# Performance work log

Measured on AMD Instinct MI355X. Metric: run time of the kernel, lower is better.

The kernel has to match this reference:

```python
import jax, jax.numpy as jnp
import numpy as np

USER_SIZE = 100000
ITEM_SIZE = 100000
EMBED = 64
BATCH = 16384
A = 0.2  # history-pooling mixing coefficient (self.a in the torch module)


def setup_inputs() -> dict:
    key = jax.random.key(0)
    ks = jax.random.split(key, 16)
    d = {}
    # index inputs
    names = ["user", "item", "pre1", "pre2", "pre3", "pre4", "pre5"]
    for i, n in enumerate(names):
        vocab = USER_SIZE if n == "user" else ITEM_SIZE
        d[n] = jax.random.randint(ks[i], (BATCH,), 0, vocab, dtype=jnp.int32)
    # embedding tables (Linear(vocab, embed) weight transposed => (vocab, embed))
    d["Wu"] = jax.random.normal(ks[7], (USER_SIZE, EMBED), jnp.float32) * (1.0 / np.sqrt(USER_SIZE + EMBED))
    d["bu"] = jnp.zeros((EMBED,), jnp.float32)
    d["Wi"] = jax.random.normal(ks[8], (ITEM_SIZE, EMBED), jnp.float32) * (1.0 / np.sqrt(ITEM_SIZE + EMBED))
    d["bi"] = jnp.zeros((EMBED,), jnp.float32)
    # MLP: 2E -> 2E -> E -> 1 (torch Linear weight layout: (out, in))
    d["W1"] = jax.random.normal(ks[9], (2 * EMBED, 2 * EMBED), jnp.float32) * (1.0 / np.sqrt(2 * EMBED))
    d["b1"] = jnp.zeros((2 * EMBED,), jnp.float32)
    d["W2"] = jax.random.normal(ks[10], (EMBED, 2 * EMBED), jnp.float32) * (1.0 / np.sqrt(2 * EMBED))
    d["b2"] = jnp.zeros((EMBED,), jnp.float32)
    d["W3"] = jax.random.normal(ks[11], (1, EMBED), jnp.float32) * (1.0 / np.sqrt(EMBED))
    d["b3"] = jnp.zeros((1,), jnp.float32)
    return d


def reference(user, item, pre1, pre2, pre3, pre4, pre5,
              Wu, bu, Wi, bi, W1, b1, W2, b2, W3, b3):
    # one-hot @ Linear == row-gather from the (vocab, embed) table + bias
    eu = jax.nn.relu(Wu[user] + bu)                     # [B, E]
    ei = jax.nn.relu(Wi[item] + bi)                     # [B, E]
    pres = jnp.stack([pre1, pre2, pre3, pre4, pre5], 1) # [B, 5]
    ep = jax.nn.relu(Wi[pres] + bi)                     # [B, 5, E]
    # attention scores: dot(item_embed, each history embed), softmax over 5
    w = jnp.einsum("be,bke->bk", ei, ep)                # [B, 5]
    z = jax.nn.softmax(w, axis=1)                       # same math as exp/sum (stable)
    pum = jnp.einsum("bk,bke->be", z, ep)               # [B, E]
    pu = eu + A * pum
    x = jnp.concatenate([pu, ei], axis=-1)              # [B, 2E]
    h = jax.nn.relu(x @ W1.T + b1)
    h = jax.nn.relu(h @ W2.T + b2)
    out = h @ W3.T + b3                                 # [B, 1]
    return jax.nn.sigmoid(out).reshape(-1)              # [B]
```

## Files before the change

### kernel.cpp

```cpp
#include <hip/hip_runtime.h>
#include <hip/hip_bf16.h>
#include <math.h>

#define EMBED 64
#define BATCH 16384
#define TB 32
#define LDX 136

typedef __attribute__((ext_vector_type(8))) short short8;
typedef __attribute__((ext_vector_type(4))) float f32x4;

__device__ inline void store_bf16x4(__hip_bfloat16* dst, float4 v) {
    __hip_bfloat16 tmp[4];
    tmp[0] = __float2bfloat16(v.x); tmp[1] = __float2bfloat16(v.y);
    tmp[2] = __float2bfloat16(v.z); tmp[3] = __float2bfloat16(v.w);
    *reinterpret_cast<ushort4*>(dst) = *reinterpret_cast<ushort4*>(tmp);
}

__device__ inline short8 load_w_bf16(const float* p) {
    const float4 lo = reinterpret_cast<const float4*>(p)[0];
    const float4 hi = reinterpret_cast<const float4*>(p)[1];
    __hip_bfloat16 tb[8];
    tb[0] = __float2bfloat16(lo.x); tb[1] = __float2bfloat16(lo.y);
    tb[2] = __float2bfloat16(lo.z); tb[3] = __float2bfloat16(lo.w);
    tb[4] = __float2bfloat16(hi.x); tb[5] = __float2bfloat16(hi.y);
    tb[6] = __float2bfloat16(hi.z); tb[7] = __float2bfloat16(hi.w);
    return *reinterpret_cast<short8*>(tb);
}

__device__ inline void attn_one(float4 eu_r, float4 ei_r, float4 ep[5],
                                float4 bu4, float4 bi4,
                                __hip_bfloat16* xrow) {
    float4 eu, ei;
    eu.x = fmaxf(eu_r.x + bu4.x, 0.0f); eu.y = fmaxf(eu_r.y + bu4.y, 0.0f);
    eu.z = fmaxf(eu_r.z + bu4.z, 0.0f); eu.w = fmaxf(eu_r.w + bu4.w, 0.0f);
    ei.x = fmaxf(ei_r.x + bi4.x, 0.0f); ei.y = fmaxf(ei_r.y + bi4.y, 0.0f);
    ei.z = fmaxf(ei_r.z + bi4.z, 0.0f); ei.w = fmaxf(ei_r.w + bi4.w, 0.0f);

    float w[5];
    #pragma unroll
    for (int k = 0; k < 5; ++k) {
        ep[k].x = fmaxf(ep[k].x + bi4.x, 0.0f);
        ep[k].y = fmaxf(ep[k].y + bi4.y, 0.0f);
        ep[k].z = fmaxf(ep[k].z + bi4.z, 0.0f);
        ep[k].w = fmaxf(ep[k].w + bi4.w, 0.0f);
        w[k] = ei.x * ep[k].x + ei.y * ep[k].y + ei.z * ep[k].z + ei.w * ep[k].w;
    }

    #pragma unroll
    for (int k = 0; k < 5; ++k) {
        float v = w[k];
        v += __shfl_xor(v, 1, 64);
        v += __shfl_xor(v, 2, 64);
        v += __shfl_xor(v, 4, 64);
        v += __shfl_xor(v, 8, 64);
        w[k] = v;
    }

    float m = w[0];
    #pragma unroll
    for (int k = 1; k < 5; ++k) m = fmaxf(m, w[k]);
    float z[5], s = 0.0f;
    #pragma unroll
    for (int k = 0; k < 5; ++k) { z[k] = __expf(w[k] - m); s += z[k]; }
    const float scale = 0.2f / s;

    float4 pum = {0.0f, 0.0f, 0.0f, 0.0f};
    #pragma unroll
    for (int k = 0; k < 5; ++k) {
        pum.x += z[k] * ep[k].x; pum.y += z[k] * ep[k].y;
        pum.z += z[k] * ep[k].z; pum.w += z[k] * ep[k].w;
    }
    float4 pu;
    pu.x = eu.x + scale * pum.x; pu.y = eu.y + scale * pum.y;
    pu.z = eu.z + scale * pum.z; pu.w = eu.w + scale * pum.w;

    const int el = (threadIdx.x & 63) & 15;
    store_bf16x4(&xrow[el * 4], pu);
    store_bf16x4(&xrow[64 + el * 4], ei);
}

__global__ __launch_bounds__(256, 2) void ncf_fused(
    const int* __restrict__ user, const int* __restrict__ item,
    const int* __restrict__ p1, const int* __restrict__ p2,
    const int* __restrict__ p3, const int* __restrict__ p4, const int* __restrict__ p5,
    const float* __restrict__ Wu, const float* __restrict__ bu,
    const float* __restrict__ Wi, const float* __restrict__ bi,
    const float* __restrict__ W1, const float* __restrict__ b1v,
    const float* __restrict__ W2, const float* __restrict__ b2v,
    const float* __restrict__ W3, const float* __restrict__ b3,
    float* __restrict__ out)
{
    __shared__ __align__(16) __hip_bfloat16 xs [TB * LDX];
    __shared__ __align__(16) __hip_bfloat16 h1s[TB * LDX];
    __shared__ __align__(16) float          h2s[TB * 68];

    const int t    = threadIdx.x;
    const int lane = t & 63;
    const int wv   = t >> 6;
    const int blk  = blockIdx.x;

    const int fr = lane & 15;
    const int kg = lane >> 4;
    const int n0 = wv * 32;
    const int n2 = wv * 16;

    const int sub = lane >> 4;
    const int el  = lane & 15;
    const int b0  = wv * 4 + sub;
    const int b1  = 16 + b0;
    const int gb0 = blk * TB + b0;
    const int gb1 = blk * TB + b1;

    const int iu0 = user[gb0], ii0 = item[gb0];
    const int iu1 = user[gb1], ii1 = item[gb1];
    int ip0[5], ip1[5];
    ip0[0] = p1[gb0]; ip0[1] = p2[gb0]; ip0[2] = p3[gb0]; ip0[3] = p4[gb0]; ip0[4] = p5[gb0];
    ip1[0] = p1[gb1]; ip1[1] = p2[gb1]; ip1[2] = p3[gb1]; ip1[3] = p4[gb1]; ip1[4] = p5[gb1];

    const float4 eu_r0 = reinterpret_cast<const float4*>(&Wu[(size_t)iu0 * EMBED])[el];
    const float4 ei_r0 = reinterpret_cast<const float4*>(&Wi[(size_t)ii0 * EMBED])[el];
    const float4 eu_r1 = reinterpret_cast<const float4*>(&Wu[(size_t)iu1 * EMBED])[el];
    const float4 ei_r1 = reinterpret_cast<const float4*>(&Wi[(size_t)ii1 * EMBED])[el];
    float4 ep0[5], ep1[5];
    #pragma unroll
    for (int k = 0; k < 5; ++k) {
        ep0[k] = reinterpret_cast<const float4*>(&Wi[(size_t)ip0[k] * EMBED])[el];
        ep1[k] = reinterpret_cast<const float4*>(&Wi[(size_t)ip1[k] * EMBED])[el];
    }

    short8 b1f[2][4];
    #pragma unroll
    for (int tile = 0; tile < 2; ++tile)
        #pragma unroll
        for (int kc = 0; kc < 4; ++kc)
            b1f[tile][kc] = load_w_bf16(&W1[(n0 + tile * 16 + fr) * 128 + kc * 32 + kg * 8]);

    const float4 bu4 = reinterpret_cast<const float4*>(bu)[el];
    const float4 bi4 = reinterpret_cast<const float4*>(bi)[el];

    attn_one(eu_r0, ei_r0, ep0, bu4, bi4, &xs[b0 * LDX]);
    attn_one(eu_r1, ei_r1, ep1, bu4, bi4, &xs[b1 * LDX]);

    __syncthreads();

    {
        const float bb0 = b1v[n0 + fr];
        const float bb1 = b1v[n0 + 16 + fr];

        #pragma unroll
        for (int mt = 0; mt < 2; ++mt) {
            short8 a[4];
            #pragma unroll
            for (int kc = 0; kc < 4; ++kc)
                a[kc] = *reinterpret_cast<const short8*>(
                    &xs[(mt * 16 + fr) * LDX + kc * 32 + kg * 8]);

            f32x4 c0 = {bb0, bb0, bb0, bb0};
            f32x4 c1 = {bb1, bb1, bb1, bb1};
            #pragma unroll
            for (int kc = 0; kc < 4; ++kc) {
                c0 = __builtin_amdgcn_mfma_f32_16x16x32_bf16(a[kc], b1f[0][kc], c0, 0, 0, 0);
                c1 = __builtin_amdgcn_mfma_f32_16x16x32_bf16(a[kc], b1f[1][kc], c1, 0, 0, 0);
            }

            #pragma unroll
            for (int r = 0; r < 4; ++r) {
                const int row = mt * 16 + kg * 4 + r;
                h1s[row * LDX + n0 + fr]      = __float2bfloat16(fmaxf(c0[r], 0.0f));
                h1s[row * LDX + n0 + 16 + fr] = __float2bfloat16(fmaxf(c1[r], 0.0f));
            }
        }
    }

    short8 b2f[4];
    #pragma unroll
    for (int kc = 0; kc < 4; ++kc)
        b2f[kc] = load_w_bf16(&W2[(n2 + fr) * 128 + kc * 32 + kg * 8]);

    __syncthreads();

    {
        const float bb2 = b2v[n2 + fr];

        #pragma unroll
        for (int mt = 0; mt < 2; ++mt) {
            short8 a2[4];
            #pragma unroll
            for (int kc = 0; kc < 4; ++kc)
                a2[kc] = *reinterpret_cast<const short8*>(
                    &h1s[(mt * 16 + fr) * LDX + kc * 32 + kg * 8]);

            f32x4 c2 = {bb2, bb2, bb2, bb2};
            #pragma unroll
            for (int kc = 0; kc < 4; ++kc)
                c2 = __builtin_amdgcn_mfma_f32_16x16x32_bf16(a2[kc], b2f[kc], c2, 0, 0, 0);

            #pragma unroll
            for (int r = 0; r < 4; ++r)
                h2s[(mt * 16 + kg * 4 + r) * 68 + n2 + fr] = fmaxf(c2[r], 0.0f);
        }
    }

    __syncthreads();

    {
        const int bl = wv * 8 + (lane >> 3);
        const int q  = lane & 7;
        const float4* w3p = reinterpret_cast<const float4*>(&W3[q * 8]);
        const float4* hp  = reinterpret_cast<const float4*>(&h2s[bl * 68 + q * 8]);
        const float4 w0 = w3p[0], w1 = w3p[1];
        const float4 h0 = hp[0],  h1 = hp[1];
        float acc = h0.x * w0.x + h0.y * w0.y + h0.z * w0.z + h0.w * w0.w
                  + h1.x * w1.x + h1.y * w1.y + h1.z * w1.z + h1.w * w1.w;
        acc += __shfl_xor(acc, 1, 64);
        acc += __shfl_xor(acc, 2, 64);
        acc += __shfl_xor(acc, 4, 64);
        if (q == 0)
            out[blk * TB + bl] = 1.0f / (1.0f + __expf(-(acc + b3[0])));
    }
}

extern "C" void kernel_launch(void* const* d_in, const int* in_sizes, int n_in,
                              void* d_out, int out_size, void* d_ws, size_t ws_size,
                              hipStream_t stream) {
    const int*   user = (const int*)  d_in[0];
    const int*   item = (const int*)  d_in[1];
    const int*   p1   = (const int*)  d_in[2];
    const int*   p2   = (const int*)  d_in[3];
    const int*   p3   = (const int*)  d_in[4];
    const int*   p4   = (const int*)  d_in[5];
    const int*   p5   = (const int*)  d_in[6];
    const float* Wu   = (const float*)d_in[7];
    const float* bu   = (const float*)d_in[8];
    const float* Wi   = (const float*)d_in[9];
    const float* bi   = (const float*)d_in[10];
    const float* W1   = (const float*)d_in[11];
    const float* b1   = (const float*)d_in[12];
    const float* W2   = (const float*)d_in[13];
    const float* b2   = (const float*)d_in[14];
    const float* W3   = (const float*)d_in[15];
    const float* b3   = (const float*)d_in[16];
    float* out = (float*)d_out;

    hipLaunchKernelGGL(ncf_fused, dim3(BATCH / TB), dim3(256), 0, stream,
                       user, item, p1, p2, p3, p4, p5,
                       Wu, bu, Wi, bi, W1, b1, W2, b2, W3, b3, out);
}
```

Before: 15.30 us.

## Double batch tile to 64 rows with 512-thread blocks and remap MFMA work

Raises the batch tile per block from 32 to 64 and the block size to 512 threads (8 waves). Each wave now computes one 16-column slice of layer 1 across four row tiles, and layer 2 is split by row tile and column pair. The aim is to amortise the per-block fp32-to-bf16 conversion of W1/W2 fragments over twice as many rows and to halve the block count. The cost is fewer blocks (256) on a large GPU, which may reduce parallelism and latency hiding during the gathers. The layer-3 section is not shown, so its mapping for 64 rows cannot be checked.

```diff
diff --git a/kernel.cpp b/kernel.cpp
--- a/kernel.cpp
+++ b/kernel.cpp
@@ -4,7 +4,7 @@
 
 #define EMBED 64
 #define BATCH 16384
-#define TB 32
+#define TB 64
 #define LDX 136
 
 typedef __attribute__((ext_vector_type(8))) short short8;
@@ -80,7 +80,7 @@
     store_bf16x4(&xrow[64 + el * 4], ei);
 }
 
-__global__ __launch_bounds__(256, 2) void ncf_fused(
+__global__ __launch_bounds__(512, 2) void ncf_fused(
     const int* __restrict__ user, const int* __restrict__ item,
     const int* __restrict__ p1, const int* __restrict__ p2,
     const int* __restrict__ p3, const int* __restrict__ p4, const int* __restrict__ p5,
@@ -102,13 +102,11 @@
 
     const int fr = lane & 15;
     const int kg = lane >> 4;
-    const int n0 = wv * 32;
-    const int n2 = wv * 16;
 
     const int sub = lane >> 4;
     const int el  = lane & 15;
     const int b0  = wv * 4 + sub;
-    const int b1  = 16 + b0;
+    const int b1  = 32 + b0;
     const int gb0 = blk * TB + b0;
     const int gb1 = blk * TB + b1;
 
@@ -129,12 +127,11 @@
         ep1[k] = reinterpret_cast<const float4*>(&Wi[(size_t)ip1[k] * EMBED])[el];
     }
 
-    short8 b1f[2][4];
-    #pragma unroll
-    for (int tile = 0; tile < 2; ++tile)
-        #pragma unroll
-        for (int kc = 0; kc < 4; ++kc)
-            b1f[tile][kc] = load_w_bf16(&W1[(n0 + tile * 16 + fr) * 128 + kc * 32 + kg * 8]);
+    const int n1 = wv * 16;
+    short8 b1f[4];
+    #pragma unroll
+    for (int kc = 0; kc < 4; ++kc)
+        b1f[kc] = load_w_bf16(&W1[(n1 + fr) * 128 + kc * 32 + kg * 8]);
 
     const float4 bu4 = reinterpret_cast<const float4*>(bu)[el];
     const float4 bi4 = reinterpret_cast<const float4*>(bi)[el];
@@ -145,60 +142,61 @@
     __syncthreads();
 
     {
-        const float bb0 = b1v[n0 + fr];
-        const float bb1 = b1v[n0 + 16 + fr];
-
-        #pragma unroll
-        for (int mt = 0; mt < 2; ++mt) {
+        const float bb = b1v[n1 + fr];
+
+        #pragma unroll
+        for (int mt = 0; mt < 4; ++mt) {
             short8 a[4];
             #pragma unroll
             for (int kc = 0; kc < 4; ++kc)
                 a[kc] = *reinterpret_cast<const short8*>(
                     &xs[(mt * 16 + fr) * LDX + kc * 32 + kg * 8]);
 
-            f32x4 c0 = {bb0, bb0, bb0, bb0};
-            f32x4 c1 = {bb1, bb1, bb1, bb1};
-            #pragma unroll
-            for (int kc = 0; kc < 4; ++kc) {
-                c0 = __builtin_amdgcn_mfma_f32_16x16x32_bf16(a[kc], b1f[0][kc], c0, 0, 0, 0);
-                c1 = __builtin_amdgcn_mfma_f32_16x16x32_bf16(a[kc], b1f[1][kc], c1, 0, 0, 0);
-            }
-
-            #pragma unroll
-            for (int r = 0; r < 4; ++r) {
-                const int row = mt * 16 + kg * 4 + r;
-                h1s[row * LDX + n0 + fr]      = __float2bfloat16(fmaxf(c0[r], 0.0f));
-                h1s[row * LDX + n0 + 16 + fr] = __float2bfloat16(fmaxf(c1[r], 0.0f));
-            }
-        }
-    }
-
-    short8 b2f[4];
-    #pragma unroll
-    for (int kc = 0; kc < 4; ++kc)
-        b2f[kc] = load_w_bf16(&W2[(n2 + fr) * 128 + kc * 32 + kg * 8]);
-
-    __syncthreads();
-
-    {
-        const float bb2 = b2v[n2 + fr];
-
-        #pragma unroll
-        for (int mt = 0; mt < 2; ++mt) {
-            short8 a2[4];
+            f32x4 c = {bb, bb, bb, bb};
             #pragma unroll
             for (int kc = 0; kc < 4; ++kc)
-                a2[kc] = *reinterpret_cast<const short8*>(
-                    &h1s[(mt * 16 + fr) * LDX + kc * 32 + kg * 8]);
-
-            f32x4 c2 = {bb2, bb2, bb2, bb2};
-            #pragma unroll
-            for (int kc = 0; kc < 4; ++kc)
-                c2 = __builtin_amdgcn_mfma_f32_16x16x32_bf16(a2[kc], b2f[kc], c2, 0, 0, 0);
+                c = __builtin_amdgcn_mfma_f32_16x16x32_bf16(a[kc], b1f[kc], c, 0, 0, 0);
 
             #pragma unroll
             for (int r = 0; r < 4; ++r)
-                h2s[(mt * 16 + kg * 4 + r) * 68 + n2 + fr] = fmaxf(c2[r], 0.0f);
+                h1s[(mt * 16 + kg * 4 + r) * LDX + n1 + fr] = __float2bfloat16(fmaxf(c[r], 0.0f));
+        }
+    }
+
+    const int mt2 = wv & 3;
+    const int nc0 = (wv >> 2) * 16;
+    const int nc1 = nc0 + 32;
+    short8 b2fa[4], b2fb[4];
+    #pragma unroll
+    for (int kc = 0; kc < 4; ++kc) {
+        b2fa[kc] = load_w_bf16(&W2[(nc0 + fr) * 128 + kc * 32 + kg * 8]);
+        b2fb[kc] = load_w_bf16(&W2[(nc1 + fr) * 128 + kc * 32 + kg * 8]);
+    }
+
+    __syncthreads();
+
+    {
+        short8 a2[4];
+        #pragma unroll
+        for (int kc = 0; kc < 4; ++kc)
+            a2[kc] = *reinterpret_cast<const short8*>(
+                &h1s[(mt2 * 16 + fr) * LDX + kc * 32 + kg * 8]);
+
+        const float bba = b2v[nc0 + fr];
+        const float bbb = b2v[nc1 + fr];
+        f32x4 ca = {bba, bba, bba, bba};
+        f32x4 cb = {bbb, bbb, bbb, bbb};
+        #pragma unroll
+        for (int kc = 0; kc < 4; ++kc) {
+            ca = __builtin_amdgcn_mfma_f32_16x16x32_bf16(a2[kc], b2fa[kc], ca, 0, 0, 0);
+            cb = __builtin_amdgcn_mfma_f32_16x16x32_bf16(a2[kc], b2fb[kc], cb, 0, 0, 0);
+        }
+
+        #pragma unroll
+        for (int r = 0; r < 4; ++r) {
+            const int row = mt2 * 16 + kg * 4 + r;
+            h2s[row * 68 + nc0 + fr] = fmaxf(ca[r], 0.0f);
+            h2s[row * 68 + nc1 + fr] = fmaxf(cb[r], 0.0f);
         }
     }
 
@@ -243,7 +241,7 @@
     const float* b3   = (const float*)d_in[16];
     float* out = (float*)d_out;
 
-    hipLaunchKernelGGL(ncf_fused, dim3(BATCH / TB), dim3(256), 0, stream,
+    hipLaunchKernelGGL(ncf_fused, dim3(BATCH / TB), dim3(512), 0, stream,
                        user, item, p1, p2, p3, p4, p5,
                        Wu, bu, Wi, bi, W1, b1, W2, b2, W3, b3, out);
 }
```

After: 15.68 us. +2.4%, slower.
